# Kernel optimization log

Hardware: AMD Instinct MI355X
Metric: run time of the kernel (lower is better)

Reference implementation:

```python
import jax, jax.numpy as jnp
import numpy as np

B = 2048          # batch_size
W = 512           # input_window_size (token feature dim)
E = 16            # n_routed_experts
K = 2             # n_activated_experts (topk)
INTER = 1024      # moe_inter_dim
SH_INTER = 2 * 1024  # n_shared_experts * inter_dim
OUT = 128         # output_window_size
ROUTE_SCALE = 1.0


def setup_inputs() -> dict:
    key = jax.random.key(0)
    ks = jax.random.split(key, 18)
    sW = 1.0 / np.sqrt(W)
    sI = 1.0 / np.sqrt(INTER)
    sS = 1.0 / np.sqrt(SH_INTER)
    return {
        "x": jax.random.normal(ks[0], (B, W), jnp.float32),
        "task_id": 0,
        # gate: F.linear(x, weight) -> no bias used in forward
        "gate_w": jax.random.normal(ks[1], (E, W), jnp.float32) * sW,
        # routed experts, stacked over E. torch Linear: y = x @ w.T + b
        "w1": jax.random.normal(ks[2], (E, INTER, W), jnp.float32) * sW,
        "b1": jax.random.normal(ks[3], (E, INTER), jnp.float32) * sW,
        "w2": jax.random.normal(ks[4], (E, W, INTER), jnp.float32) * sI,
        "b2": jax.random.normal(ks[5], (E, W), jnp.float32) * sI,
        "w3": jax.random.normal(ks[6], (E, INTER, W), jnp.float32) * sW,
        "b3": jax.random.normal(ks[7], (E, INTER), jnp.float32) * sW,
        # shared expert (SwiGLU-like MLP on the window dim)
        "sw1": jax.random.normal(ks[8], (SH_INTER, W), jnp.float32) * sW,
        "sb1": jax.random.normal(ks[9], (SH_INTER,), jnp.float32) * sW,
        "sw2": jax.random.normal(ks[10], (W, SH_INTER), jnp.float32) * sS,
        "sb2": jax.random.normal(ks[11], (W,), jnp.float32) * sS,
        "sw3": jax.random.normal(ks[12], (SH_INTER, W), jnp.float32) * sW,
        "sb3": jax.random.normal(ks[13], (SH_INTER,), jnp.float32) * sW,
        # output layer
        "ow": jax.random.normal(ks[14], (OUT, W), jnp.float32) * sW,
        "ob": jax.random.normal(ks[15], (OUT,), jnp.float32) * sW,
    }


def reference(x, task_id, gate_w, w1, b1, w2, b2, w3, b3,
              sw1, sb1, sw2, sb2, sw3, sb3, ow, ob):
    xf = x.reshape(x.shape[0], -1)                      # [B, W]
    b = xf.shape[0]

    # --- gate: softmax scores, top-k routing weights ---
    scores = jax.nn.softmax(xf @ gate_w.T, axis=-1)     # [B, E] (fp32 softmax)
    top_w, top_i = jax.lax.top_k(scores, K)             # [B, K]
    top_w = (top_w * ROUTE_SCALE).astype(xf.dtype)
    # dense combine weights: zero except selected experts (topk indices distinct)
    combine = jnp.zeros((b, E), xf.dtype).at[jnp.arange(b)[:, None], top_i].add(top_w)

    # --- routed experts (dense, all experts on all tokens, masked combine) ---
    h1 = jnp.einsum('bw,eiw->bei', xf, w1) + b1          # [B, E, INTER]
    h3 = jnp.einsum('bw,eiw->bei', xf, w3) + b3
    h = jax.nn.leaky_relu(h1) * h3                       # leaky_relu slope 0.01
    eo = jnp.einsum('bei,ewi->bew', h, w2) + b2          # [B, E, W]
    y = jnp.einsum('bew,be->bw', eo, combine)            # weighted combine

    # --- shared expert ---
    z = (jax.nn.leaky_relu(xf @ sw1.T + sb1) * (xf @ sw3.T + sb3)) @ sw2.T + sb2

    out = (y + z) @ ow.T + ob                            # [B, OUT]
    return out.reshape(B, OUT)
```

## Files before the change

### kernel.cpp

```cpp
#include <hip/hip_runtime.h>

#define B_TOK 2048
#define W_DIM 512
#define E_N 16
#define INTER 1024
#define SH_INTER 2048
#define OUT_DIM 128

typedef unsigned short u16;
typedef unsigned int u32;
typedef __attribute__((ext_vector_type(8))) short bf16x8;
typedef __attribute__((ext_vector_type(4))) float f32x4;

__device__ __forceinline__ u16 f2b(float f) {
    union { float f; unsigned u; } x; x.f = f;
    unsigned r = x.u + 0x7FFFu + ((x.u >> 16) & 1u);
    return (u16)(r >> 16);
}

__device__ __forceinline__ u32 cvtpk(float lo, float hi) {
    u32 r;
    asm("v_cvt_pk_bf16_f32 %0, %1, %2" : "=v"(r) : "v"(lo), "v"(hi));
    return r;
}

__device__ __forceinline__ void gld16(const void* g, void* l) {
    __builtin_amdgcn_global_load_lds(
        (const __attribute__((address_space(1))) void*)g,
        (__attribute__((address_space(3))) void*)l, 16, 0, 0);
}


struct CastSeg { const float4* src; uint4* dst; int n8; };
struct CastArgs { CastSeg s[8]; };

__global__ __launch_bounds__(256)
void cast_all(CastArgs a) {
    int rem = blockIdx.x * 2048;
    int s = 0;
    while (rem >= a.s[s].n8) { rem -= a.s[s].n8; ++s; }
    const float4* __restrict__ src = a.s[s].src + (size_t)rem * 2;
    uint4* __restrict__ dst = a.s[s].dst + rem;
    const int t = threadIdx.x;
    float4 v[16];
    #pragma unroll
    for (int k = 0; k < 8; ++k) {
        v[2 * k]     = src[(size_t)(t + k * 256) * 2];
        v[2 * k + 1] = src[(size_t)(t + k * 256) * 2 + 1];
    }
    #pragma unroll
    for (int k = 0; k < 8; ++k) {
        uint4 o;
        o.x = cvtpk(v[2 * k].x,     v[2 * k].y);
        o.y = cvtpk(v[2 * k].z,     v[2 * k].w);
        o.z = cvtpk(v[2 * k + 1].x, v[2 * k + 1].y);
        o.w = cvtpk(v[2 * k + 1].z, v[2 * k + 1].w);
        dst[t + k * 256] = o;
    }
}

__global__ __launch_bounds__(256)
void gate_topk(const float* __restrict__ x, const float* __restrict__ gw,
               int* __restrict__ topi, float* __restrict__ topw) {
    const int lane = threadIdx.x & 63;
    const int wv   = threadIdx.x >> 6;
    const int t    = blockIdx.x * 4 + wv;
    const int e = lane >> 2, q = lane & 3;
    const float4* xr = (const float4*)(x + (size_t)t * W_DIM);
    const float4* wr = (const float4*)(gw + (size_t)e * W_DIM);
    float s = 0.f;
    #pragma unroll
    for (int i = 0; i < W_DIM / 16; ++i) {
        float4 a = xr[q + 4 * i];
        float4 b = wr[q + 4 * i];
        s += a.x * b.x + a.y * b.y + a.z * b.z + a.w * b.w;
    }
    s += __shfl_xor(s, 1);
    s += __shfl_xor(s, 2);
    float sc[16];
    #pragma unroll
    for (int ee = 0; ee < 16; ++ee) sc[ee] = __shfl(s, ee * 4);
    float mx = sc[0];
    #pragma unroll
    for (int ee = 1; ee < 16; ++ee) mx = fmaxf(mx, sc[ee]);
    float p[16]; float sum = 0.f;
    #pragma unroll
    for (int ee = 0; ee < 16; ++ee) { p[ee] = expf(sc[ee] - mx); sum += p[ee]; }
    const float inv = 1.f / sum;
    int i0 = 0; float v0 = sc[0];
    #pragma unroll
    for (int ee = 1; ee < 16; ++ee) if (sc[ee] > v0) { v0 = sc[ee]; i0 = ee; }
    int i1 = -1; float v1 = -1e30f;
    #pragma unroll
    for (int ee = 0; ee < 16; ++ee) if (ee != i0 && sc[ee] > v1) { v1 = sc[ee]; i1 = ee; }
    if (lane == 0) {
        topi[t * 2 + 0] = i0; topi[t * 2 + 1] = i1;
        topw[t * 2 + 0] = p[i0] * inv; topw[t * 2 + 1] = p[i1] * inv;
    }
}

__global__ __launch_bounds__(256)
void route_build(const int* __restrict__ topi, const float* __restrict__ topw,
                 int* __restrict__ meta, int* __restrict__ glist,
                 float* __restrict__ job_w, int* __restrict__ t2r) {
    __shared__ int cnt[16], cur[16], offs[16];
    const int tid = threadIdx.x;
    if (tid < 16) { cnt[tid] = 0; cur[tid] = 0; }
    __syncthreads();
    for (int i = tid; i < 2 * B_TOK; i += 256) atomicAdd(&cnt[topi[i]], 1);
    __syncthreads();
    if (tid == 0) {
        int acc = 0, jc = 0;
        for (int e = 0; e < 16; ++e) {
            offs[e] = acc; meta[e] = cnt[e]; meta[32 + e] = acc; acc += cnt[e];
        }
        for (int e = 0; e < 16; ++e)
            for (int m = 0; m < cnt[e]; m += 128) { meta[64 + jc] = e; meta[128 + jc] = m; ++jc; }
        for (int m = 0; m < B_TOK; m += 128) { meta[64 + jc] = 16; meta[128 + jc] = m; ++jc; }
        meta[50] = jc;
        jc = 0;
        for (int e = 0; e < 16; ++e)
            for (int m = 0; m < cnt[e]; m += 64) { meta[192 + jc] = e; meta[304 + jc] = m; ++jc; }
        for (int m = 0; m < B_TOK; m += 64) { meta[192 + jc] = 16; meta[304 + jc] = m; ++jc; }
        meta[51] = jc;
    }
    __syncthreads();
    for (int i = tid; i < 2 * B_TOK; i += 256) {
        int e = topi[i];
        int pos = atomicAdd(&cur[e], 1);
        int row = offs[e] + pos;
        glist[row] = i >> 1;
        job_w[row] = topw[i];
        t2r[i] = row;
    }
    for (int t = tid; t < B_TOK; t += 256) glist[4096 + t] = t;
}

__global__ __launch_bounds__(256)
void g1_dual(const u16* __restrict__ xb, const int* __restrict__ glist, const int* __restrict__ meta,
             const u16* __restrict__ w1b, const u16* __restrict__ w3b,
             const float* __restrict__ b1, const float* __restrict__ b3,
             const u16* __restrict__ sw1b, const u16* __restrict__ sw3b,
             const float* __restrict__ sb1, const float* __restrict__ sb3,
             u16* __restrict__ hbuf, u16* __restrict__ pbuf) {
    const int job = blockIdx.x;
    if (job >= meta[50]) return;
    const int e  = meta[64 + job];
    const int m0 = meta[128 + job];
    const bool sh = (e == 16);
    if (!sh && blockIdx.y >= (INTER / 64)) return;
    const int n0 = blockIdx.y * 64;
    const int N  = sh ? SH_INTER : INTER;
    const u16* B1 = sh ? sw1b : (w1b + (size_t)e * INTER * W_DIM);
    const u16* B3 = sh ? sw3b : (w3b + (size_t)e * INTER * W_DIM);
    const float* bb1 = sh ? sb1 : (b1 + (size_t)e * INTER);
    const float* bb3 = sh ? sb3 : (b3 + (size_t)e * INTER);
    const int abase = sh ? (4096 + m0) : (meta[32 + e] + m0);
    const int Mrows = (sh ? B_TOK : meta[e]) - m0;
    u16* outp = sh ? pbuf : hbuf;
    const int orow0 = sh ? m0 : (meta[32 + e] + m0);

    __shared__ __align__(16) u16 lds[2 * 8192];

    const int tid = threadIdx.x, lane = tid & 63, wv = tid >> 6;
    const int rA0 = tid >> 2, rA1 = rA0 + 64;
    const int kq = (tid & 3) * 8;
    const int tok0 = glist[abase + (rA0 < Mrows ? rA0 : Mrows - 1)];
    const int tok1 = glist[abase + (rA1 < Mrows ? rA1 : Mrows - 1)];
    const u16* gA0 = xb + (size_t)tok0 * W_DIM + kq;
    const u16* gA1 = xb + (size_t)tok1 * W_DIM + kq;
    const u16* gB1 = B1 + (size_t)(n0 + rA0) * W_DIM + kq;
    const u16* gB3 = B3 + (size_t)(n0 + rA0) * W_DIM + kq;

    const int wm = wv >> 1, wn = wv & 1;
    const int l15 = lane & 15, lhi = lane >> 4;

    f32x4 a1[4][2] = {};
    f32x4 a3[4][2] = {};

    auto stage = [&](int s, int k0) {
        u16* b = &lds[s * 8192];
        gld16(gA0 + k0, b + tid * 8);
        gld16(gA1 + k0, b + 2048 + tid * 8);
        gld16(gB1 + k0, b + 4096 + tid * 8);
        gld16(gB3 + k0, b + 6144 + tid * 8);
    };

    const int NT = W_DIM / 32;
    int cur = 0;
    stage(0, 0);
    for (int t = 0; t < NT; ++t) {
        __syncthreads();
        if (t + 1 < NT) stage(cur ^ 1, (t + 1) * 32);
        const u16* bb = &lds[cur * 8192];
        bf16x8 af[4], f1[2], f3[2];
        #pragma unroll
        for (int i = 0; i < 4; ++i)
            af[i] = *(const bf16x8*)&bb[(wm * 64 + i * 16 + l15) * 32 + lhi * 8];
        #pragma unroll
        for (int j = 0; j < 2; ++j) {
            f1[j] = *(const bf16x8*)&bb[4096 + (wn * 32 + j * 16 + l15) * 32 + lhi * 8];
            f3[j] = *(const bf16x8*)&bb[6144 + (wn * 32 + j * 16 + l15) * 32 + lhi * 8];
        }
        #pragma unroll
        for (int i = 0; i < 4; ++i)
            #pragma unroll
            for (int j = 0; j < 2; ++j) {
                a1[i][j] = __builtin_amdgcn_mfma_f32_16x16x32_bf16(af[i], f1[j], a1[i][j], 0, 0, 0);
                a3[i][j] = __builtin_amdgcn_mfma_f32_16x16x32_bf16(af[i], f3[j], a3[i][j], 0, 0, 0);
            }
        cur ^= 1;
    }

    #pragma unroll
    for (int i = 0; i < 4; ++i)
    #pragma unroll
    for (int j = 0; j < 2; ++j) {
        const int col = n0 + wn * 32 + j * 16 + l15;
        const float vb1 = bb1[col];
        const float vb3 = bb3[col];
        #pragma unroll
        for (int r = 0; r < 4; ++r) {
            const int gm = wm * 64 + i * 16 + lhi * 4 + r;
            if (gm < Mrows) {
                float v1 = a1[i][j][r] + vb1;
                float v3 = a3[i][j][r] + vb3;
                v1 = v1 >= 0.f ? v1 : 0.01f * v1;
                outp[(size_t)(orow0 + gm) * N + col] = f2b(v1 * v3);
            }
        }
    }
}

__global__ __launch_bounds__(256)
void g2_gemm(const int* __restrict__ meta,
             const u16* __restrict__ hbuf, const u16* __restrict__ pbuf,
             const u16* __restrict__ w2b, const float* __restrict__ b2,
             const u16* __restrict__ sw2b, const float* __restrict__ sb2,
             const float* __restrict__ job_w,
             float* __restrict__ y2, float* __restrict__ zbuf) {
    const int job = blockIdx.x;
    if (job >= meta[51]) return;
    const int e  = meta[192 + job];
    const int m0 = meta[304 + job];
    const bool sh = (e == 16);
    const int n0 = blockIdx.y * 64;
    const int K  = sh ? SH_INTER : INTER;
    const u16* A = sh ? pbuf : hbuf;
    const int Arow0 = sh ? m0 : (meta[32 + e] + m0);
    const u16* Bw = sh ? sw2b : (w2b + (size_t)e * W_DIM * INTER);
    const float* bias = sh ? sb2 : (b2 + (size_t)e * W_DIM);
    const int Mrows = (sh ? B_TOK : meta[e]) - m0;
    const float* scale = sh ? nullptr : (job_w + Arow0);
    float* outp = sh ? zbuf : y2;

    __shared__ __align__(16) u16 lds[2 * 4096];

    const int tid = threadIdx.x, lane = tid & 63, wv = tid >> 6;
    const int rA = tid >> 2;
    const int kq = (tid & 3) * 8;
    const u16* gA = A + (size_t)(Arow0 + (rA < Mrows ? rA : Mrows - 1)) * K + kq;
    const u16* gB = Bw + (size_t)(n0 + rA) * K + kq;

    const int wm = wv >> 1, wn = wv & 1;
    const int l15 = lane & 15, lhi = lane >> 4;

    f32x4 acc[2][2] = {};

    auto stage = [&](int s, int k0) {
        u16* b = &lds[s * 4096];
        gld16(gA + k0, b + tid * 8);
        gld16(gB + k0, b + 2048 + tid * 8);
    };

    const int NT = K / 32;
    int cur = 0;
    stage(0, 0);
    for (int t = 0; t < NT; ++t) {
        __syncthreads();
        if (t + 1 < NT) stage(cur ^ 1, (t + 1) * 32);
        const u16* bb = &lds[cur * 4096];
        bf16x8 af[2], bf[2];
        #pragma unroll
        for (int i = 0; i < 2; ++i)
            af[i] = *(const bf16x8*)&bb[(wm * 32 + i * 16 + l15) * 32 + lhi * 8];
        #pragma unroll
        for (int j = 0; j < 2; ++j)
            bf[j] = *(const bf16x8*)&bb[2048 + (wn * 32 + j * 16 + l15) * 32 + lhi * 8];
        #pragma unroll
        for (int i = 0; i < 2; ++i)
            #pragma unroll
            for (int j = 0; j < 2; ++j)
                acc[i][j] = __builtin_amdgcn_mfma_f32_16x16x32_bf16(af[i], bf[j], acc[i][j], 0, 0, 0);
        cur ^= 1;
    }

    #pragma unroll
    for (int i = 0; i < 2; ++i)
    #pragma unroll
    for (int j = 0; j < 2; ++j) {
        const int col = n0 + wn * 32 + j * 16 + l15;
        const float bb = bias[col];
        #pragma unroll
        for (int r = 0; r < 4; ++r) {
            const int gm = wm * 32 + i * 16 + lhi * 4 + r;
            if (gm < Mrows) {
                float v = acc[i][j][r] + bb;
                if (scale) v *= scale[gm];
                outp[(size_t)(Arow0 + gm) * W_DIM + col] = v;
            }
        }
    }
}

__global__ __launch_bounds__(256)
void combine_k(const float* __restrict__ y2, const float* __restrict__ z,
               const int* __restrict__ t2r, u16* __restrict__ ybf) {
    int idx = blockIdx.x * 256 + threadIdx.x;
    int t = idx >> 7;
    int w4 = (idx & 127) << 2;
    int r0 = t2r[t * 2 + 0], r1 = t2r[t * 2 + 1];
    const float4 a = *(const float4*)(y2 + (size_t)r0 * W_DIM + w4);
    const float4 b = *(const float4*)(y2 + (size_t)r1 * W_DIM + w4);
    const float4 c = *(const float4*)(z + (size_t)t * W_DIM + w4);
    ushort4 o;
    o.x = f2b(a.x + b.x + c.x);
    o.y = f2b(a.y + b.y + c.y);
    o.z = f2b(a.z + b.z + c.z);
    o.w = f2b(a.w + b.w + c.w);
    *(ushort4*)(ybf + (size_t)t * W_DIM + w4) = o;
}

__global__ __launch_bounds__(256)
void gout(const u16* __restrict__ ybf, const u16* __restrict__ owb,
          const float* __restrict__ ob, float* __restrict__ out) {
    const int m0 = blockIdx.x * 64, n0 = blockIdx.y * 64;
    __shared__ __align__(16) u16 lds[2 * 4096];
    const int tid = threadIdx.x, lane = tid & 63, wv = tid >> 6;
    const int rA = tid >> 2;
    const int kq = (tid & 3) * 8;
    const u16* gA = ybf + (size_t)(m0 + rA) * W_DIM + kq;
    const u16* gB = owb + (size_t)(n0 + rA) * W_DIM + kq;
    const int wm = wv >> 1, wn = wv & 1;
    const int l15 = lane & 15, lhi = lane >> 4;
    f32x4 acc[2][2] = {};
    auto stage = [&](int s, int k0) {
        u16* b = &lds[s * 4096];
        gld16(gA + k0, b + tid * 8);
        gld16(gB + k0, b + 2048 + tid * 8);
    };
    const int NT = W_DIM / 32;
    int cur = 0;
    stage(0, 0);
    for (int t = 0; t < NT; ++t) {
        __syncthreads();
        if (t + 1 < NT) stage(cur ^ 1, (t + 1) * 32);
        const u16* bb = &lds[cur * 4096];
        bf16x8 af[2], bf[2];
        #pragma unroll
        for (int i = 0; i < 2; ++i)
            af[i] = *(const bf16x8*)&bb[(wm * 32 + i * 16 + l15) * 32 + lhi * 8];
        #pragma unroll
        for (int j = 0; j < 2; ++j)
            bf[j] = *(const bf16x8*)&bb[2048 + (wn * 32 + j * 16 + l15) * 32 + lhi * 8];
        #pragma unroll
        for (int i = 0; i < 2; ++i)
            #pragma unroll
            for (int j = 0; j < 2; ++j)
                acc[i][j] = __builtin_amdgcn_mfma_f32_16x16x32_bf16(af[i], bf[j], acc[i][j], 0, 0, 0);
        cur ^= 1;
    }
    #pragma unroll
    for (int i = 0; i < 2; ++i)
    #pragma unroll
    for (int j = 0; j < 2; ++j) {
        const int col = n0 + wn * 32 + j * 16 + l15;
        if (col < OUT_DIM) {
            const float bb = ob[col];
            #pragma unroll
            for (int r = 0; r < 4; ++r) {
                const int gm = wm * 32 + i * 16 + lhi * 4 + r;
                out[(size_t)(m0 + gm) * OUT_DIM + col] = acc[i][j][r] + bb;
            }
        }
    }
}

extern "C" void kernel_launch(void* const* d_in, const int* in_sizes, int n_in,
                              void* d_out, int out_size, void* d_ws, size_t ws_size,
                              hipStream_t stream) {
    const float* x      = (const float*)d_in[0];
    const float* gate_w = (const float*)d_in[2];
    const float* w1     = (const float*)d_in[3];
    const float* b1     = (const float*)d_in[4];
    const float* w2     = (const float*)d_in[5];
    const float* b2     = (const float*)d_in[6];
    const float* w3     = (const float*)d_in[7];
    const float* b3     = (const float*)d_in[8];
    const float* sw1    = (const float*)d_in[9];
    const float* sb1    = (const float*)d_in[10];
    const float* sw2    = (const float*)d_in[11];
    const float* sb2    = (const float*)d_in[12];
    const float* sw3    = (const float*)d_in[13];
    const float* sb3    = (const float*)d_in[14];
    const float* ow     = (const float*)d_in[15];
    const float* ob     = (const float*)d_in[16];
    float* out = (float*)d_out;

    char* ws = (char*)d_ws;
    size_t off = 0;
    auto alloc = [&](size_t bytes) -> void* {
        void* p = (void*)(ws + off);
        off += (bytes + 255) & ~(size_t)255;
        return p;
    };

    int*   meta   = (int*)alloc(2048);
    int*   topi   = (int*)alloc((size_t)B_TOK * 2 * 4);
    float* topw   = (float*)alloc((size_t)B_TOK * 2 * 4);
    int*   t2r    = (int*)alloc((size_t)B_TOK * 2 * 4);
    int*   glist  = (int*)alloc((size_t)(B_TOK * 2 + B_TOK) * 4);
    float* job_w  = (float*)alloc((size_t)B_TOK * 2 * 4);
    u16*   xb     = (u16*)alloc((size_t)B_TOK * W_DIM * 2);
    u16*   w1b    = (u16*)alloc((size_t)E_N * INTER * W_DIM * 2);
    u16*   w3b    = (u16*)alloc((size_t)E_N * INTER * W_DIM * 2);
    u16*   w2b    = (u16*)alloc((size_t)E_N * W_DIM * INTER * 2);
    u16*   sw1b   = (u16*)alloc((size_t)SH_INTER * W_DIM * 2);
    u16*   sw3b   = (u16*)alloc((size_t)SH_INTER * W_DIM * 2);
    u16*   sw2b   = (u16*)alloc((size_t)W_DIM * SH_INTER * 2);
    u16*   owb    = (u16*)alloc((size_t)OUT_DIM * W_DIM * 2);
    u16*   hbuf   = (u16*)alloc((size_t)B_TOK * 2 * INTER * 2);
    u16*   pbuf   = (u16*)alloc((size_t)B_TOK * SH_INTER * 2);
    float* y2     = (float*)alloc((size_t)B_TOK * 2 * W_DIM * 4);
    float* zbuf   = (float*)alloc((size_t)B_TOK * W_DIM * 4);
    u16*   ybf    = (u16*)alloc((size_t)B_TOK * W_DIM * 2);
    if (off > ws_size) return;

    dim3 blk(256);

    CastArgs ca;
    ca.s[0] = { (const float4*)x,   (uint4*)xb,   B_TOK * W_DIM / 8 };
    ca.s[1] = { (const float4*)w1,  (uint4*)w1b,  E_N * INTER * W_DIM / 8 };
    ca.s[2] = { (const float4*)w3,  (uint4*)w3b,  E_N * INTER * W_DIM / 8 };
    ca.s[3] = { (const float4*)w2,  (uint4*)w2b,  E_N * W_DIM * INTER / 8 };
    ca.s[4] = { (const float4*)sw1, (uint4*)sw1b, SH_INTER * W_DIM / 8 };
    ca.s[5] = { (const float4*)sw3, (uint4*)sw3b, SH_INTER * W_DIM / 8 };
    ca.s[6] = { (const float4*)sw2, (uint4*)sw2b, W_DIM * SH_INTER / 8 };
    ca.s[7] = { (const float4*)ow,  (uint4*)owb,  OUT_DIM * W_DIM / 8 };
    int total8 = 0;
    for (int i = 0; i < 8; ++i) total8 += ca.s[i].n8;
    cast_all<<<dim3(total8 / 2048), blk, 0, stream>>>(ca);

    gate_topk<<<dim3(B_TOK / 4), blk, 0, stream>>>(x, gate_w, topi, topw);
    route_build<<<1, blk, 0, stream>>>(topi, topw, meta, glist, job_w, t2r);

    g1_dual<<<dim3(64, SH_INTER / 64), blk, 0, stream>>>(
        xb, glist, meta, w1b, w3b, b1, b3, sw1b, sw3b, sb1, sb3, hbuf, pbuf);

    g2_gemm<<<dim3(112, W_DIM / 64), blk, 0, stream>>>(
        meta, hbuf, pbuf, w2b, b2, sw2b, sb2, job_w, y2, zbuf);

    combine_k<<<dim3(B_TOK * W_DIM / 4 / 256), blk, 0, stream>>>(y2, zbuf, t2r, ybf);

    gout<<<dim3(B_TOK / 64, 2), blk, 0, stream>>>(ybf, owb, ob, out);
}
```

Measured before the change: 133.3 us.

## Fuse fp32-to-bf16 weight conversion into GEMM B-tile loads with register prefetch

```diff
diff --git a/kernel.cpp b/kernel.cpp
--- a/kernel.cpp
+++ b/kernel.cpp
@@ -12,6 +12,10 @@
 typedef __attribute__((ext_vector_type(8))) short bf16x8;
 typedef __attribute__((ext_vector_type(4))) float f32x4;
 
+#define WAITV(N) asm volatile("s_waitcnt vmcnt(" #N ")" ::: "memory")
+#define WAITL()  asm volatile("s_waitcnt lgkmcnt(0)" ::: "memory")
+#define SBAR()   __builtin_amdgcn_s_barrier()
+
 __device__ __forceinline__ u16 f2b(float f) {
     union { float f; unsigned u; } x; x.f = f;
     unsigned r = x.u + 0x7FFFu + ((x.u >> 16) & 1u);
@@ -32,29 +36,25 @@
 
 
 struct CastSeg { const float4* src; uint4* dst; int n8; };
-struct CastArgs { CastSeg s[8]; };
-
-__global__ __launch_bounds__(256)
-void cast_all(CastArgs a) {
+struct CastArgs { CastSeg s[2]; };
+
+__global__ __launch_bounds__(256)
+void cast_small(CastArgs a) {
     int rem = blockIdx.x * 2048;
     int s = 0;
     while (rem >= a.s[s].n8) { rem -= a.s[s].n8; ++s; }
     const float4* __restrict__ src = a.s[s].src + (size_t)rem * 2;
     uint4* __restrict__ dst = a.s[s].dst + rem;
     const int t = threadIdx.x;
-    float4 v[16];
     #pragma unroll
     for (int k = 0; k < 8; ++k) {
-        v[2 * k]     = src[(size_t)(t + k * 256) * 2];
-        v[2 * k + 1] = src[(size_t)(t + k * 256) * 2 + 1];
-    }
-    #pragma unroll
-    for (int k = 0; k < 8; ++k) {
+        float4 v0 = src[(size_t)(t + k * 256) * 2];
+        float4 v1 = src[(size_t)(t + k * 256) * 2 + 1];
         uint4 o;
-        o.x = cvtpk(v[2 * k].x,     v[2 * k].y);
-        o.y = cvtpk(v[2 * k].z,     v[2 * k].w);
-        o.z = cvtpk(v[2 * k + 1].x, v[2 * k + 1].y);
-        o.w = cvtpk(v[2 * k + 1].z, v[2 * k + 1].w);
+        o.x = cvtpk(v0.x, v0.y);
+        o.y = cvtpk(v0.z, v0.w);
+        o.z = cvtpk(v1.x, v1.y);
+        o.w = cvtpk(v1.z, v1.w);
         dst[t + k * 256] = o;
     }
 }
@@ -136,11 +136,13 @@
     for (int t = tid; t < B_TOK; t += 256) glist[4096 + t] = t;
 }
 
+struct BReg { float4 a1, b1, a3, b3; };
+
 __global__ __launch_bounds__(256)
 void g1_dual(const u16* __restrict__ xb, const int* __restrict__ glist, const int* __restrict__ meta,
-             const u16* __restrict__ w1b, const u16* __restrict__ w3b,
+             const float* __restrict__ w1, const float* __restrict__ w3,
              const float* __restrict__ b1, const float* __restrict__ b3,
-             const u16* __restrict__ sw1b, const u16* __restrict__ sw3b,
+             const float* __restrict__ sw1, const float* __restrict__ sw3,
              const float* __restrict__ sb1, const float* __restrict__ sb3,
              u16* __restrict__ hbuf, u16* __restrict__ pbuf) {
     const int job = blockIdx.x;
@@ -151,8 +153,8 @@
     if (!sh && blockIdx.y >= (INTER / 64)) return;
     const int n0 = blockIdx.y * 64;
     const int N  = sh ? SH_INTER : INTER;
-    const u16* B1 = sh ? sw1b : (w1b + (size_t)e * INTER * W_DIM);
-    const u16* B3 = sh ? sw3b : (w3b + (size_t)e * INTER * W_DIM);
+    const float* B1 = sh ? sw1 : (w1 + (size_t)e * INTER * W_DIM);
+    const float* B3 = sh ? sw3 : (w3 + (size_t)e * INTER * W_DIM);
     const float* bb1 = sh ? sb1 : (b1 + (size_t)e * INTER);
     const float* bb3 = sh ? sb3 : (b3 + (size_t)e * INTER);
     const int abase = sh ? (4096 + m0) : (meta[32 + e] + m0);
@@ -169,8 +171,8 @@
     const int tok1 = glist[abase + (rA1 < Mrows ? rA1 : Mrows - 1)];
     const u16* gA0 = xb + (size_t)tok0 * W_DIM + kq;
     const u16* gA1 = xb + (size_t)tok1 * W_DIM + kq;
-    const u16* gB1 = B1 + (size_t)(n0 + rA0) * W_DIM + kq;
-    const u16* gB3 = B3 + (size_t)(n0 + rA0) * W_DIM + kq;
+    const float* gB1 = B1 + (size_t)(n0 + rA0) * W_DIM + kq;
+    const float* gB3 = B3 + (size_t)(n0 + rA0) * W_DIM + kq;
 
     const int wm = wv >> 1, wn = wv & 1;
     const int l15 = lane & 15, lhi = lane >> 4;
@@ -178,29 +180,56 @@
     f32x4 a1[4][2] = {};
     f32x4 a3[4][2] = {};
 
-    auto stage = [&](int s, int k0) {
-        u16* b = &lds[s * 8192];
-        gld16(gA0 + k0, b + tid * 8);
-        gld16(gA1 + k0, b + 2048 + tid * 8);
-        gld16(gB1 + k0, b + 4096 + tid * 8);
-        gld16(gB3 + k0, b + 6144 + tid * 8);
+    BReg r0, r1;
+
+    auto loadB = [&](BReg& r, int k0) {
+        r.a1 = *(const float4*)(gB1 + k0);
+        r.b1 = *(const float4*)(gB1 + k0 + 4);
+        r.a3 = *(const float4*)(gB3 + k0);
+        r.b3 = *(const float4*)(gB3 + k0 + 4);
+    };
+    auto writeB = [&](const BReg& r, u16* buf) {
+        uint4 o1, o3;
+        o1.x = cvtpk(r.a1.x, r.a1.y); o1.y = cvtpk(r.a1.z, r.a1.w);
+        o1.z = cvtpk(r.b1.x, r.b1.y); o1.w = cvtpk(r.b1.z, r.b1.w);
+        o3.x = cvtpk(r.a3.x, r.a3.y); o3.y = cvtpk(r.a3.z, r.a3.w);
+        o3.z = cvtpk(r.b3.x, r.b3.y); o3.w = cvtpk(r.b3.z, r.b3.w);
+        *(uint4*)(buf + 4096 + tid * 8) = o1;
+        *(uint4*)(buf + 6144 + tid * 8) = o3;
+    };
+    auto stageA = [&](u16* buf, int k0) {
+        gld16(gA0 + k0, buf + tid * 8);
+        gld16(gA1 + k0, buf + 2048 + tid * 8);
     };
 
     const int NT = W_DIM / 32;
     int cur = 0;
-    stage(0, 0);
-    for (int t = 0; t < NT; ++t) {
-        __syncthreads();
-        if (t + 1 < NT) stage(cur ^ 1, (t + 1) * 32);
-        const u16* bb = &lds[cur * 8192];
+
+    stageA(lds, 0);
+    loadB(r0, 0);
+    WAITV(0);
+    writeB(r0, lds);
+    loadB(r1, 32);
+    WAITL();
+    SBAR();
+
+    auto step = [&](int t, BReg& rcons, BReg& rfill) {
+        u16* bufc = lds + cur * 8192;
+        u16* bufn = lds + (cur ^ 1) * 8192;
+        if (t + 1 < NT) stageA(bufn, (t + 1) * 32);
+        if (t + 2 < NT) loadB(rfill, (t + 2) * 32);
         bf16x8 af[4], f1[2], f3[2];
         #pragma unroll
         for (int i = 0; i < 4; ++i)
-            af[i] = *(const bf16x8*)&bb[(wm * 64 + i * 16 + l15) * 32 + lhi * 8];
+            af[i] = *(const bf16x8*)&bufc[(wm * 64 + i * 16 + l15) * 32 + lhi * 8];
         #pragma unroll
         for (int j = 0; j < 2; ++j) {
-            f1[j] = *(const bf16x8*)&bb[4096 + (wn * 32 + j * 16 + l15) * 32 + lhi * 8];
-            f3[j] = *(const bf16x8*)&bb[6144 + (wn * 32 + j * 16 + l15) * 32 + lhi * 8];
+            f1[j] = *(const bf16x8*)&bufc[4096 + (wn * 32 + j * 16 + l15) * 32 + lhi * 8];
+            f3[j] = *(const bf16x8*)&bufc[6144 + (wn * 32 + j * 16 + l15) * 32 + lhi * 8];
+        }
+        if (t + 1 < NT) {
+            if (t + 2 < NT) { WAITV(6); } else { WAITV(2); }
+            writeB(rcons, bufn);
         }
         #pragma unroll
         for (int i = 0; i < 4; ++i)
@@ -209,8 +238,13 @@
                 a1[i][j] = __builtin_amdgcn_mfma_f32_16x16x32_bf16(af[i], f1[j], a1[i][j], 0, 0, 0);
                 a3[i][j] = __builtin_amdgcn_mfma_f32_16x16x32_bf16(af[i], f3[j], a3[i][j], 0, 0, 0);
             }
+        if (t + 2 < NT) { WAITV(4); } else { WAITV(0); }
+        WAITL();
+        SBAR();
         cur ^= 1;
-    }
+    };
+
+    for (int t = 0; t < NT; t += 2) { step(t, r1, r0); step(t + 1, r0, r1); }
 
     #pragma unroll
     for (int i = 0; i < 4; ++i)
@@ -232,11 +266,13 @@
     }
 }
 
+struct BReg2 { float4 a, b; };
+
 __global__ __launch_bounds__(256)
 void g2_gemm(const int* __restrict__ meta,
              const u16* __restrict__ hbuf, const u16* __restrict__ pbuf,
-             const u16* __restrict__ w2b, const float* __restrict__ b2,
-             const u16* __restrict__ sw2b, const float* __restrict__ sb2,
+             const float* __restrict__ w2, const float* __restrict__ b2,
+             const float* __restrict__ sw2, const float* __restrict__ sb2,
              const float* __restrict__ job_w,
              float* __restrict__ y2, float* __restrict__ zbuf) {
     const int job = blockIdx.x;
@@ -248,7 +284,7 @@
     const int K  = sh ? SH_INTER : INTER;
     const u16* A = sh ? pbuf : hbuf;
     const int Arow0 = sh ? m0 : (meta[32 + e] + m0);
-    const u16* Bw = sh ? sw2b : (w2b + (size_t)e * W_DIM * INTER);
+    const float* Bw = sh ? sw2 : (w2 + (size_t)e * W_DIM * INTER);
     const float* bias = sh ? sb2 : (b2 + (size_t)e * W_DIM);
     const int Mrows = (sh ? B_TOK : meta[e]) - m0;
     const float* scale = sh ? nullptr : (job_w + Arow0);
@@ -259,41 +295,66 @@
     const int tid = threadIdx.x, lane = tid & 63, wv = tid >> 6;
     const int rA = tid >> 2;
     const int kq = (tid & 3) * 8;
-    const u16* gA = A + (size_t)(Arow0 + (rA < Mrows ? rA : Mrows - 1)) * K + kq;
-    const u16* gB = Bw + (size_t)(n0 + rA) * K + kq;
+    const u16*   gA = A + (size_t)(Arow0 + (rA < Mrows ? rA : Mrows - 1)) * K + kq;
+    const float* gB = Bw + (size_t)(n0 + rA) * K + kq;
 
     const int wm = wv >> 1, wn = wv & 1;
     const int l15 = lane & 15, lhi = lane >> 4;
 
     f32x4 acc[2][2] = {};
 
-    auto stage = [&](int s, int k0) {
-        u16* b = &lds[s * 4096];
-        gld16(gA + k0, b + tid * 8);
-        gld16(gB + k0, b + 2048 + tid * 8);
-    };
+    BReg2 r0, r1;
+    auto loadB = [&](BReg2& r, int k0) {
+        r.a = *(const float4*)(gB + k0);
+        r.b = *(const float4*)(gB + k0 + 4);
+    };
+    auto writeB = [&](const BReg2& r, u16* buf) {
+        uint4 o;
+        o.x = cvtpk(r.a.x, r.a.y); o.y = cvtpk(r.a.z, r.a.w);
+        o.z = cvtpk(r.b.x, r.b.y); o.w = cvtpk(r.b.z, r.b.w);
+        *(uint4*)(buf + 2048 + tid * 8) = o;
+    };
+    auto stageA = [&](u16* buf, int k0) { gld16(gA + k0, buf + tid * 8); };
 
     const int NT = K / 32;
     int cur = 0;
-    stage(0, 0);
-    for (int t = 0; t < NT; ++t) {
-        __syncthreads();
-        if (t + 1 < NT) stage(cur ^ 1, (t + 1) * 32);
-        const u16* bb = &lds[cur * 4096];
+
+    stageA(lds, 0);
+    loadB(r0, 0);
+    WAITV(0);
+    writeB(r0, lds);
+    loadB(r1, 32);
+    WAITL();
+    SBAR();
+
+    auto step = [&](int t, BReg2& rcons, BReg2& rfill) {
+        u16* bufc = lds + cur * 4096;
+        u16* bufn = lds + (cur ^ 1) * 4096;
+        if (t + 1 < NT) stageA(bufn, (t + 1) * 32);
+        if (t + 2 < NT) loadB(rfill, (t + 2) * 32);
         bf16x8 af[2], bf[2];
         #pragma unroll
         for (int i = 0; i < 2; ++i)
-            af[i] = *(const bf16x8*)&bb[(wm * 32 + i * 16 + l15) * 32 + lhi * 8];
+            af[i] = *(const bf16x8*)&bufc[(wm * 32 + i * 16 + l15) * 32 + lhi * 8];
         #pragma unroll
         for (int j = 0; j < 2; ++j)
-            bf[j] = *(const bf16x8*)&bb[2048 + (wn * 32 + j * 16 + l15) * 32 + lhi * 8];
+            bf[j] = *(const bf16x8*)&bufc[2048 + (wn * 32 + j * 16 + l15) * 32 + lhi * 8];
+        if (t + 1 < NT) {
+            if (t + 2 < NT) { WAITV(3); } else { WAITV(1); }
+            writeB(rcons, bufn);
+        }
         #pragma unroll
         for (int i = 0; i < 2; ++i)
             #pragma unroll
             for (int j = 0; j < 2; ++j)
                 acc[i][j] = __builtin_amdgcn_mfma_f32_16x16x32_bf16(af[i], bf[j], acc[i][j], 0, 0, 0);
+        if (t + 2 < NT) { WAITV(2); } else { WAITV(0); }
+        WAITL();
+        SBAR();
         cur ^= 1;
-    }
+    };
+
+    for (int t = 0; t < NT; t += 2) { step(t, r1, r0); step(t + 1, r0, r1); }
 
     #pragma unroll
     for (int i = 0; i < 2; ++i)
@@ -422,12 +483,6 @@
     int*   glist  = (int*)alloc((size_t)(B_TOK * 2 + B_TOK) * 4);
     float* job_w  = (float*)alloc((size_t)B_TOK * 2 * 4);
     u16*   xb     = (u16*)alloc((size_t)B_TOK * W_DIM * 2);
-    u16*   w1b    = (u16*)alloc((size_t)E_N * INTER * W_DIM * 2);
-    u16*   w3b    = (u16*)alloc((size_t)E_N * INTER * W_DIM * 2);
-    u16*   w2b    = (u16*)alloc((size_t)E_N * W_DIM * INTER * 2);
-    u16*   sw1b   = (u16*)alloc((size_t)SH_INTER * W_DIM * 2);
-    u16*   sw3b   = (u16*)alloc((size_t)SH_INTER * W_DIM * 2);
-    u16*   sw2b   = (u16*)alloc((size_t)W_DIM * SH_INTER * 2);
     u16*   owb    = (u16*)alloc((size_t)OUT_DIM * W_DIM * 2);
     u16*   hbuf   = (u16*)alloc((size_t)B_TOK * 2 * INTER * 2);
     u16*   pbuf   = (u16*)alloc((size_t)B_TOK * SH_INTER * 2);
@@ -439,26 +494,19 @@
     dim3 blk(256);
 
     CastArgs ca;
-    ca.s[0] = { (const float4*)x,   (uint4*)xb,   B_TOK * W_DIM / 8 };
-    ca.s[1] = { (const float4*)w1,  (uint4*)w1b,  E_N * INTER * W_DIM / 8 };
-    ca.s[2] = { (const float4*)w3,  (uint4*)w3b,  E_N * INTER * W_DIM / 8 };
-    ca.s[3] = { (const float4*)w2,  (uint4*)w2b,  E_N * W_DIM * INTER / 8 };
-    ca.s[4] = { (const float4*)sw1, (uint4*)sw1b, SH_INTER * W_DIM / 8 };
-    ca.s[5] = { (const float4*)sw3, (uint4*)sw3b, SH_INTER * W_DIM / 8 };
-    ca.s[6] = { (const float4*)sw2, (uint4*)sw2b, W_DIM * SH_INTER / 8 };
-    ca.s[7] = { (const float4*)ow,  (uint4*)owb,  OUT_DIM * W_DIM / 8 };
-    int total8 = 0;
-    for (int i = 0; i < 8; ++i) total8 += ca.s[i].n8;
-    cast_all<<<dim3(total8 / 2048), blk, 0, stream>>>(ca);
+    ca.s[0] = { (const float4*)x,  (uint4*)xb,  B_TOK * W_DIM / 8 };
+    ca.s[1] = { (const float4*)ow, (uint4*)owb, OUT_DIM * W_DIM / 8 };
+    const int total8 = B_TOK * W_DIM / 8 + OUT_DIM * W_DIM / 8;
+    cast_small<<<dim3(total8 / 2048), blk, 0, stream>>>(ca);
 
     gate_topk<<<dim3(B_TOK / 4), blk, 0, stream>>>(x, gate_w, topi, topw);
     route_build<<<1, blk, 0, stream>>>(topi, topw, meta, glist, job_w, t2r);
 
     g1_dual<<<dim3(64, SH_INTER / 64), blk, 0, stream>>>(
-        xb, glist, meta, w1b, w3b, b1, b3, sw1b, sw3b, sb1, sb3, hbuf, pbuf);
+        xb, glist, meta, w1, w3, b1, b3, sw1, sw3, sb1, sb3, hbuf, pbuf);
 
     g2_gemm<<<dim3(112, W_DIM / 64), blk, 0, stream>>>(
-        meta, hbuf, pbuf, w2b, b2, sw2b, sb2, job_w, y2, zbuf);
+        meta, hbuf, pbuf, w2, b2, sw2, sb2, job_w, y2, zbuf);
 
     combine_k<<<dim3(B_TOK * W_DIM / 4 / 256), blk, 0, stream>>>(y2, zbuf, t2r, ybf);
 
```

Result: slower. 140.0 us (+5.1%).
